# Performance work log

Measured on AMD Instinct MI355X. Metric: run time of the kernel, lower is better.

Reference implementation:

```python
import jax, jax.numpy as jnp
import numpy as np
from jax import lax

B, S, D, T = 64, 256, 1024, 60
HIST = 20  # last-20 window of attn / decoder-state history


def setup_inputs() -> dict:
    key = jax.random.key(0)
    ks = jax.random.split(key, 8)
    e_outputs = jax.random.normal(ks[0], (B, S, D), jnp.float32)
    queries = jax.random.normal(ks[1], (B, T, D), jnp.float32)
    # attention weights over source frames: rows sum to 1
    attns = jax.nn.softmax(jax.random.normal(ks[2], (B, T, S), jnp.float32), axis=-1)
    g = 0.02
    Wr = jax.random.normal(ks[3], (D, 1), jnp.float32) * g
    br = jnp.zeros((1,), jnp.float32)
    Wa = jax.random.normal(ks[4], (D, 1), jnp.float32) * g
    ba = jnp.zeros((1,), jnp.float32)
    Wq = jax.random.normal(ks[5], (D, D), jnp.float32) / np.sqrt(D)
    Wn = jax.random.normal(ks[6], (2 * D, 1), jnp.float32) * g
    bn = jnp.zeros((1,), jnp.float32)
    return {"e_outputs": e_outputs, "queries": queries, "attns": attns,
            "Wr": Wr, "br": br, "Wa": Wa, "ba": ba, "Wq": Wq, "Wn": Wn, "bn": bn}


def reference(e_outputs, queries, attns, Wr, br, Wa, ba, Wq, Wn, bn):
    Bn, Sn, Dn = e_outputs.shape
    # decay1[i] = (i+1)/20 ; decay2[i] = 1-(i+1)/50, zero-padded past 50 frames
    decay1 = (jnp.arange(HIST, dtype=jnp.float32) + 1.0) / 20.0
    idx = jnp.arange(Sn, dtype=jnp.float32)
    add0 = jnp.where(idx < 50, 1.0 - (idx + 1.0) / 50.0, 0.0)
    add_state0 = add0[None, :, None]                       # [1,S,1]
    mem0 = e_outputs * add_state0                          # [B,S,D]
    abuf0 = jnp.zeros((HIST, Bn, Sn), e_outputs.dtype)
    qbuf0 = jnp.zeros((HIST, Bn, Dn), e_outputs.dtype)

    def step(carry, x):
        mem, add_state, abuf, qbuf, i = carry
        attn_i, q_i = x                                    # [B,S], [B,D]
        # read: selected frame before memory update
        sel = jnp.einsum('bs,bsd->bd', attn_i, mem)
        # roll history buffers (newest at slot HIST-1)
        abuf = jnp.concatenate([abuf[1:], attn_i[None]], axis=0)
        qbuf = jnp.concatenate([qbuf[1:], q_i[None]], axis=0)
        k = jnp.minimum(i + 1, HIST)
        valid = jnp.arange(HIST) >= (HIST - k)
        temp = jax.nn.softmax(jnp.where(valid, decay1, -jnp.inf))
        attn_w = jnp.einsum('t,tbs->bs', temp, abuf)       # decayed attn sum
        query_s = jnp.einsum('t,tbd->bd', temp, qbuf)      # decayed query sum
        remove_prob = jax.nn.sigmoid(q_i @ Wr + br)[:, :, None]   # [B,1,1]
        add_prob = jax.nn.sigmoid(q_i @ Wa + ba)[:, :, None]      # [B,1,1]
        sim = jax.nn.sigmoid(jnp.einsum('bsd,bd->bs', mem, query_s @ Wq))[..., None]
        mem = mem * (1.0 - remove_prob * attn_w[..., None] * sim)
        last_ctx = jnp.einsum('bs,bsd->bd', attn_w, e_outputs)[:, None, :]
        cat = jnp.concatenate([e_outputs, jnp.broadcast_to(last_ctx, e_outputs.shape)], axis=-1)
        nxt = jax.nn.sigmoid(cat @ Wn + bn)                # [B,S,1]
        mem = mem + e_outputs * (1.0 - add_state) * (add_prob * nxt)
        add_state = add_state + (1.0 - add_state) * (add_prob * nxt)
        return (mem, add_state, abuf, qbuf, i + 1), sel

    init = (mem0, jnp.broadcast_to(add_state0, (Bn, Sn, 1)), abuf0, qbuf0, jnp.int32(0))
    xs = (attns.transpose(1, 0, 2), queries.transpose(1, 0, 2))
    _, sels = lax.scan(step, init, xs)
    return sels.transpose(1, 0, 2)                         # [B,T,D]
```

## Files before the change

### kernel.cpp

```cpp
#include <hip/hip_runtime.h>
#include <math.h>


#define Bn 64
#define Sn 256
#define Dn 1024
#define Tn 60
#define HISTn 20
#define LDK 72

typedef __bf16 bf16x8 __attribute__((ext_vector_type(8)));
typedef float f32x4 __attribute__((ext_vector_type(4)));
typedef unsigned short us8 __attribute__((ext_vector_type(8)));

__device__ __forceinline__ unsigned short f2bf(float f){
  unsigned int x; __builtin_memcpy(&x,&f,4);
  unsigned int lsb = (x >> 16) & 1u;
  x += 0x7fffu + lsb;
  return (unsigned short)(x >> 16);
}
__device__ __forceinline__ float sigmoidf_(float x){ return 1.0f/(1.0f+expf(-x)); }

__global__ __launch_bounds__(256) void conv_q(
    const float* __restrict__ Q, const float* __restrict__ Wr,
    const float* __restrict__ br, const float* __restrict__ Wa,
    const float* __restrict__ ba, float* __restrict__ rp,
    float* __restrict__ ap, unsigned short* __restrict__ Qbf)
{
  int row = blockIdx.x, tid = threadIdx.x;
  float4 x = ((const float4*)(Q + (size_t)row*Dn))[tid];
  float4 a = ((const float4*)Wr)[tid];
  float4 b = ((const float4*)Wa)[tid];
  unsigned short o[4] = {f2bf(x.x), f2bf(x.y), f2bf(x.z), f2bf(x.w)};
  *(uint2*)&Qbf[(size_t)row*Dn + tid*4] = *(uint2*)o;
  float s1 = x.x*a.x + x.y*a.y + x.z*a.z + x.w*a.w;
  float s2 = x.x*b.x + x.y*b.y + x.z*b.z + x.w*b.w;
  for (int off = 32; off; off >>= 1){
    s1 += __shfl_down(s1, off, 64);
    s2 += __shfl_down(s2, off, 64);
  }
  __shared__ float r1[4], r2[4];
  int lane = tid & 63, wv = tid >> 6;
  if (lane == 0){ r1[wv] = s1; r2[wv] = s2; }
  __syncthreads();
  if (tid == 0){
    rp[row] = sigmoidf_(r1[0]+r1[1]+r1[2]+r1[3] + br[0]);
    ap[row] = sigmoidf_(r2[0]+r2[1]+r2[2]+r2[3] + ba[0]);
  }
}

__global__ __launch_bounds__(256) void conv_wt(
    const float* __restrict__ Wq, unsigned short* __restrict__ WT)
{
  __shared__ __align__(16) unsigned short Tt[64][LDK];
  int n0 = blockIdx.x*64, k0 = blockIdx.y*64;
  int tid = threadIdx.x;
  int kl = tid >> 4, nl4 = (tid & 15)*4;
  #pragma unroll
  for (int it = 0; it < 4; it++){
    int k = kl + it*16;
    float4 v = *(const float4*)&Wq[(size_t)(k0+k)*Dn + n0 + nl4];
    Tt[nl4+0][k] = f2bf(v.x); Tt[nl4+1][k] = f2bf(v.y);
    Tt[nl4+2][k] = f2bf(v.z); Tt[nl4+3][k] = f2bf(v.w);
  }
  __syncthreads();
  int nr = tid >> 2, kg = (tid & 3)*16;
  *(us8*)&WT[(size_t)(n0+nr)*Dn + k0+kg]   = *(us8*)&Tt[nr][kg];
  *(us8*)&WT[(size_t)(n0+nr)*Dn + k0+kg+8] = *(us8*)&Tt[nr][kg+8];
}

__global__ __launch_bounds__(256) void gemm_qw(
    const unsigned short* __restrict__ Qbf,
    const unsigned short* __restrict__ WT,
    unsigned short* __restrict__ QWbf)
{
  __shared__ __align__(16) unsigned short As[64][LDK], Bs[64][LDK];
  int m0 = blockIdx.x*64, n0 = blockIdx.y*64;
  int tid = threadIdx.x, lane = tid & 63, wave = tid >> 6;
  int quad = lane >> 4, l16 = lane & 15;
  f32x4 acc[4];
  #pragma unroll
  for (int nt=0;nt<4;nt++)
    #pragma unroll
    for (int r=0;r<4;r++) acc[nt][r]=0.f;
  int sr = tid >> 2, sk = (tid & 3)*16;
  for (int k0 = 0; k0 < Dn; k0 += 64){
    *(us8*)&As[sr][sk]   = *(const us8*)&Qbf[(size_t)(m0+sr)*Dn + k0+sk];
    *(us8*)&As[sr][sk+8] = *(const us8*)&Qbf[(size_t)(m0+sr)*Dn + k0+sk+8];
    *(us8*)&Bs[sr][sk]   = *(const us8*)&WT[(size_t)(n0+sr)*Dn + k0+sk];
    *(us8*)&Bs[sr][sk+8] = *(const us8*)&WT[(size_t)(n0+sr)*Dn + k0+sk+8];
    __syncthreads();
    #pragma unroll
    for (int kk = 0; kk < 64; kk += 32){
      bf16x8 a = *(const bf16x8*)&As[wave*16 + l16][kk + quad*8];
      #pragma unroll
      for (int nt=0;nt<4;nt++){
        bf16x8 bb = *(const bf16x8*)&Bs[nt*16 + l16][kk + quad*8];
        acc[nt] = __builtin_amdgcn_mfma_f32_16x16x32_bf16(a, bb, acc[nt], 0, 0, 0);
      }
    }
    __syncthreads();
  }
  #pragma unroll
  for (int nt=0;nt<4;nt++)
    #pragma unroll
    for (int r=0;r<4;r++){
      int m = m0 + wave*16 + quad*4 + r;
      int n = n0 + nt*16 + l16;
      QWbf[(size_t)m*Dn + n] = f2bf(acc[nt][r]);
    }
}

__global__ __launch_bounds__(256) void gemm_g(
    const unsigned short* __restrict__ QWbf,
    const float* __restrict__ E,
    const float* __restrict__ Wn,
    float* __restrict__ G, float* __restrict__ eW1, float* __restrict__ eW2)
{
  __shared__ __align__(16) unsigned short As[64][LDK], Bs[32][LDK];
  int b = blockIdx.x, n0 = blockIdx.y*32;
  int tid = threadIdx.x, lane = tid & 63, wave = tid >> 6;
  int quad = lane >> 4, l16 = lane & 15;
  f32x4 acc[2];
  #pragma unroll
  for (int nt=0;nt<2;nt++)
    #pragma unroll
    for (int r=0;r<4;r++) acc[nt][r]=0.f;
  int sr = tid >> 2, sk = (tid & 3)*16;
  int br = tid >> 3, bk = (tid & 7)*8;
  float d1 = 0.f, d2 = 0.f;
  for (int k0 = 0; k0 < Dn; k0 += 64){
    if (sr < Tn){
      *(us8*)&As[sr][sk]   = *(const us8*)&QWbf[((size_t)(b*Tn + sr))*Dn + k0+sk];
      *(us8*)&As[sr][sk+8] = *(const us8*)&QWbf[((size_t)(b*Tn + sr))*Dn + k0+sk+8];
    } else {
      us8 z = (us8)0;
      *(us8*)&As[sr][sk] = z; *(us8*)&As[sr][sk+8] = z;
    }
    const float* ep = &E[((size_t)(b*Sn + n0 + br))*Dn + k0 + bk];
    float4 e0 = *(const float4*)ep;
    float4 e1 = *(const float4*)(ep+4);
    const float* w1 = &Wn[k0 + bk];
    const float* w2 = &Wn[Dn + k0 + bk];
    float4 w10 = *(const float4*)w1, w11 = *(const float4*)(w1+4);
    float4 w20 = *(const float4*)w2, w21 = *(const float4*)(w2+4);
    d1 += e0.x*w10.x + e0.y*w10.y + e0.z*w10.z + e0.w*w10.w
        + e1.x*w11.x + e1.y*w11.y + e1.z*w11.z + e1.w*w11.w;
    d2 += e0.x*w20.x + e0.y*w20.y + e0.z*w20.z + e0.w*w20.w
        + e1.x*w21.x + e1.y*w21.y + e1.z*w21.z + e1.w*w21.w;
    unsigned short cv[8] = {f2bf(e0.x), f2bf(e0.y), f2bf(e0.z), f2bf(e0.w),
                            f2bf(e1.x), f2bf(e1.y), f2bf(e1.z), f2bf(e1.w)};
    *(us8*)&Bs[br][bk] = *(us8*)cv;
    __syncthreads();
    #pragma unroll
    for (int kk = 0; kk < 64; kk += 32){
      bf16x8 a = *(const bf16x8*)&As[wave*16 + l16][kk + quad*8];
      #pragma unroll
      for (int nt=0;nt<2;nt++){
        bf16x8 bb = *(const bf16x8*)&Bs[nt*16 + l16][kk + quad*8];
        acc[nt] = __builtin_amdgcn_mfma_f32_16x16x32_bf16(a, bb, acc[nt], 0, 0, 0);
      }
    }
    __syncthreads();
  }
  d1 += __shfl_down(d1, 4, 64); d1 += __shfl_down(d1, 2, 64); d1 += __shfl_down(d1, 1, 64);
  d2 += __shfl_down(d2, 4, 64); d2 += __shfl_down(d2, 2, 64); d2 += __shfl_down(d2, 1, 64);
  if ((tid & 7) == 0){
    eW1[b*Sn + n0 + br] = d1;
    eW2[b*Sn + n0 + br] = d2;
  }
  #pragma unroll
  for (int nt=0;nt<2;nt++)
    #pragma unroll
    for (int r=0;r<4;r++){
      int t = wave*16 + quad*4 + r;
      int s = n0 + nt*16 + l16;
      if (t < Tn) G[((size_t)(b*Tn + t))*Sn + s] = acc[nt][r];
    }
}

__global__ __launch_bounds__(256) void kR_lc(
    const float* __restrict__ At,
    const float* __restrict__ eW2,
    float* __restrict__ lc)
{
  int b = blockIdx.x, tid = threadIdx.x;
  int lane = tid & 63, wv = tid >> 6;
  __shared__ float Rsh[Tn];
  float4 e2v = ((const float4*)(eW2 + (size_t)b*Sn))[lane];
  const float* at_b = At + (size_t)b*Tn*Sn;
  #pragma unroll
  for (int w = 0; w < 15; w++){
    int j = wv + w*4;
    float4 a4 = ((const float4*)(at_b + (size_t)j*Sn))[lane];
    float v = a4.x*e2v.x + a4.y*e2v.y + a4.z*e2v.z + a4.w*e2v.w;
    #pragma unroll
    for (int off = 32; off; off >>= 1) v += __shfl_down(v, off, 64);
    if (lane == 0) Rsh[j] = v;
  }
  __syncthreads();
  if (tid < Tn){
    int i = tid;
    int j0 = (i - HISTn + 1 > 0) ? i - HISTn + 1 : 0;
    float num = 0.f, den = 0.f;
    for (int j = j0; j <= i; j++){
      float wj = expf(0.05f*(j+1));
      num += wj * Rsh[j];
      den += wj;
    }
    lc[b*Tn + i] = num / den;
  }
}

__global__ __launch_bounds__(256) void scan_m(
    const float* __restrict__ At,
    const float* __restrict__ G,
    const float* __restrict__ rp,
    const float* __restrict__ ap,
    const float* __restrict__ eW1,
    const float* __restrict__ lc,
    const float* __restrict__ bnp,
    unsigned short* __restrict__ Pbf)
{
  int b = blockIdx.x, s = threadIdx.x;
  float M = (s < 50) ? (1.0f - (s+1)/50.0f) : 0.0f;
  float A = M;
  float bnv = bnp[0];
  float e1 = eW1[b*Sn + s];
  const float* at_b = At + (size_t)b*Tn*Sn + s;
  const float* G_b  = G  + (size_t)b*Tn*Sn + s;
  unsigned short* P_b = Pbf + (size_t)b*Tn*Sn + s;
  const float* lc_b = lc + b*Tn;
  const float* rp_b = rp + b*Tn;
  const float* ap_b = ap + b*Tn;
  float num_a = 0.f, num_q = 0.f, den = 0.f;
  #pragma unroll
  for (int i = 0; i < Tn; i++){
    float wi = expf(0.05f*(i+1));
    float a_new = at_b[i*Sn];
    float g_new = G_b[i*Sn];
    num_a += wi * a_new;
    num_q += wi * g_new;
    den   += wi;
    if (i >= HISTn){
      float wo = expf(0.05f*(i-HISTn+1));
      num_a -= wo * at_b[(i-HISTn)*Sn];
      num_q -= wo * G_b[(i-HISTn)*Sn];
      den   -= wo;
    }
    float inv = 1.0f / den;
    float aw = num_a * inv;
    float qd = num_q * inv;
    P_b[i*Sn] = f2bf(a_new * M);
    float sim = sigmoidf_(M * qd);
    float nxt = sigmoidf_(e1 + lc_b[i] + bnv);
    M = M * (1.0f - rp_b[i] * aw * sim);
    float g = (1.0f - A) * ap_b[i] * nxt;
    M += g; A += g;
  }
}

__global__ __launch_bounds__(256) void gemm_sels(
    const unsigned short* __restrict__ Pbf,
    const float* __restrict__ E,
    float* __restrict__ out)
{
  __shared__ __align__(16) unsigned short As[64][LDK], Bs[64][LDK];
  int b = blockIdx.x, n0 = blockIdx.y*64;
  int tid = threadIdx.x, lane = tid & 63, wave = tid >> 6;
  int quad = lane >> 4, l16 = lane & 15;
  f32x4 acc[4];
  #pragma unroll
  for (int nt=0;nt<4;nt++)
    #pragma unroll
    for (int r=0;r<4;r++) acc[nt][r]=0.f;
  int sr = tid >> 2, sk = (tid & 3)*16;
  for (int k0 = 0; k0 < Sn; k0 += 64){
    if (sr < Tn){
      *(us8*)&As[sr][sk]   = *(const us8*)&Pbf[((size_t)(b*Tn + sr))*Sn + k0+sk];
      *(us8*)&As[sr][sk+8] = *(const us8*)&Pbf[((size_t)(b*Tn + sr))*Sn + k0+sk+8];
    } else {
      us8 z = (us8)0;
      *(us8*)&As[sr][sk] = z; *(us8*)&As[sr][sk+8] = z;
    }
    {
      const float* ep = &E[((size_t)(b*Sn + k0 + sr))*Dn + n0 + sk];
      float4 e0 = *(const float4*)ep;
      float4 e1 = *(const float4*)(ep+4);
      float4 e2 = *(const float4*)(ep+8);
      float4 e3 = *(const float4*)(ep+12);
      float ev[16] = {e0.x,e0.y,e0.z,e0.w, e1.x,e1.y,e1.z,e1.w,
                      e2.x,e2.y,e2.z,e2.w, e3.x,e3.y,e3.z,e3.w};
      #pragma unroll
      for (int j=0;j<16;j++) Bs[sk+j][sr] = f2bf(ev[j]);
    }
    __syncthreads();
    #pragma unroll
    for (int kk = 0; kk < 64; kk += 32){
      bf16x8 a = *(const bf16x8*)&As[wave*16 + l16][kk + quad*8];
      #pragma unroll
      for (int nt=0;nt<4;nt++){
        bf16x8 bb = *(const bf16x8*)&Bs[nt*16 + l16][kk + quad*8];
        acc[nt] = __builtin_amdgcn_mfma_f32_16x16x32_bf16(a, bb, acc[nt], 0, 0, 0);
      }
    }
    __syncthreads();
  }
  #pragma unroll
  for (int nt=0;nt<4;nt++)
    #pragma unroll
    for (int r=0;r<4;r++){
      int t = wave*16 + quad*4 + r;
      int d = n0 + nt*16 + l16;
      if (t < Tn) out[((size_t)(b*Tn + t))*Dn + d] = acc[nt][r];
    }
}

extern "C" void kernel_launch(void* const* d_in, const int* in_sizes, int n_in,
                              void* d_out, int out_size, void* d_ws, size_t ws_size,
                              hipStream_t stream)
{
  const float* E  = (const float*)d_in[0];
  const float* Q  = (const float*)d_in[1];
  const float* At = (const float*)d_in[2];
  const float* Wr = (const float*)d_in[3];
  const float* br = (const float*)d_in[4];
  const float* Wa = (const float*)d_in[5];
  const float* ba = (const float*)d_in[6];
  const float* Wq = (const float*)d_in[7];
  const float* Wn = (const float*)d_in[8];
  const float* bnp= (const float*)d_in[9];

  char* ws = (char*)d_ws;
  float* rp  = (float*)ws; ws += (size_t)Bn*Tn*4;
  float* ap  = (float*)ws; ws += (size_t)Bn*Tn*4;
  float* eW1 = (float*)ws; ws += (size_t)Bn*Sn*4;
  float* eW2 = (float*)ws; ws += (size_t)Bn*Sn*4;
  float* lc  = (float*)ws; ws += (size_t)Bn*Tn*4;
  unsigned short* Qbf  = (unsigned short*)ws; ws += (size_t)Bn*Tn*Dn*2;
  unsigned short* WT   = (unsigned short*)ws; ws += (size_t)Dn*Dn*2;
  unsigned short* QWbf = (unsigned short*)ws; ws += (size_t)Bn*Tn*Dn*2;
  float* G = (float*)ws; ws += (size_t)Bn*Tn*Sn*4;
  unsigned short* Pbf = (unsigned short*)ws; ws += (size_t)Bn*Tn*Sn*2;

  conv_q<<<Bn*Tn, 256, 0, stream>>>(Q, Wr, br, Wa, ba, rp, ap, Qbf);
  conv_wt<<<dim3(16,16), 256, 0, stream>>>(Wq, WT);
  gemm_qw<<<dim3(Bn*Tn/64, Dn/64), 256, 0, stream>>>(Qbf, WT, QWbf);
  gemm_g<<<dim3(Bn, Sn/32), 256, 0, stream>>>(QWbf, E, Wn, G, eW1, eW2);
  kR_lc<<<Bn, 256, 0, stream>>>(At, eW2, lc);
  scan_m<<<Bn, 256, 0, stream>>>(At, G, rp, ap, eW1, lc, bnp, Pbf);
  gemm_sels<<<dim3(Bn, Dn/64), 256, 0, stream>>>(Pbf, E, (float*)d_out);
}
```

Before: 220.3 us.

## Pre-convert E to bf16 once and fuse small prep kernels

```diff
diff --git a/kernel.cpp b/kernel.cpp
--- a/kernel.cpp
+++ b/kernel.cpp
@@ -13,6 +13,9 @@
 typedef float f32x4 __attribute__((ext_vector_type(4)));
 typedef unsigned short us8 __attribute__((ext_vector_type(8)));
 
+__device__ __forceinline__ float bf2f(unsigned short u){
+  unsigned int x = ((unsigned int)u) << 16; float f; __builtin_memcpy(&f,&x,4); return f;
+}
 __device__ __forceinline__ unsigned short f2bf(float f){
   unsigned int x; __builtin_memcpy(&x,&f,4);
   unsigned int lsb = (x >> 16) & 1u;
@@ -21,52 +24,61 @@
 }
 __device__ __forceinline__ float sigmoidf_(float x){ return 1.0f/(1.0f+expf(-x)); }
 
-__global__ __launch_bounds__(256) void conv_q(
+__global__ __launch_bounds__(256) void conv_qw(
     const float* __restrict__ Q, const float* __restrict__ Wr,
     const float* __restrict__ br, const float* __restrict__ Wa,
-    const float* __restrict__ ba, float* __restrict__ rp,
-    float* __restrict__ ap, unsigned short* __restrict__ Qbf)
-{
-  int row = blockIdx.x, tid = threadIdx.x;
-  float4 x = ((const float4*)(Q + (size_t)row*Dn))[tid];
-  float4 a = ((const float4*)Wr)[tid];
-  float4 b = ((const float4*)Wa)[tid];
-  unsigned short o[4] = {f2bf(x.x), f2bf(x.y), f2bf(x.z), f2bf(x.w)};
-  *(uint2*)&Qbf[(size_t)row*Dn + tid*4] = *(uint2*)o;
-  float s1 = x.x*a.x + x.y*a.y + x.z*a.z + x.w*a.w;
-  float s2 = x.x*b.x + x.y*b.y + x.z*b.z + x.w*b.w;
-  for (int off = 32; off; off >>= 1){
-    s1 += __shfl_down(s1, off, 64);
-    s2 += __shfl_down(s2, off, 64);
-  }
-  __shared__ float r1[4], r2[4];
-  int lane = tid & 63, wv = tid >> 6;
-  if (lane == 0){ r1[wv] = s1; r2[wv] = s2; }
-  __syncthreads();
-  if (tid == 0){
-    rp[row] = sigmoidf_(r1[0]+r1[1]+r1[2]+r1[3] + br[0]);
-    ap[row] = sigmoidf_(r2[0]+r2[1]+r2[2]+r2[3] + ba[0]);
-  }
-}
-
-__global__ __launch_bounds__(256) void conv_wt(
-    const float* __restrict__ Wq, unsigned short* __restrict__ WT)
-{
-  __shared__ __align__(16) unsigned short Tt[64][LDK];
-  int n0 = blockIdx.x*64, k0 = blockIdx.y*64;
+    const float* __restrict__ ba, const float* __restrict__ Wq,
+    float* __restrict__ rp, float* __restrict__ ap,
+    unsigned short* __restrict__ Qbf, unsigned short* __restrict__ WT)
+{
   int tid = threadIdx.x;
-  int kl = tid >> 4, nl4 = (tid & 15)*4;
-  #pragma unroll
-  for (int it = 0; it < 4; it++){
-    int k = kl + it*16;
-    float4 v = *(const float4*)&Wq[(size_t)(k0+k)*Dn + n0 + nl4];
-    Tt[nl4+0][k] = f2bf(v.x); Tt[nl4+1][k] = f2bf(v.y);
-    Tt[nl4+2][k] = f2bf(v.z); Tt[nl4+3][k] = f2bf(v.w);
-  }
-  __syncthreads();
-  int nr = tid >> 2, kg = (tid & 3)*16;
-  *(us8*)&WT[(size_t)(n0+nr)*Dn + k0+kg]   = *(us8*)&Tt[nr][kg];
-  *(us8*)&WT[(size_t)(n0+nr)*Dn + k0+kg+8] = *(us8*)&Tt[nr][kg+8];
+  if (blockIdx.x < Bn*Tn){
+    int row = blockIdx.x;
+    float4 x = ((const float4*)(Q + (size_t)row*Dn))[tid];
+    float4 a = ((const float4*)Wr)[tid];
+    float4 b = ((const float4*)Wa)[tid];
+    unsigned short o[4] = {f2bf(x.x), f2bf(x.y), f2bf(x.z), f2bf(x.w)};
+    *(uint2*)&Qbf[(size_t)row*Dn + tid*4] = *(uint2*)o;
+    float s1 = x.x*a.x + x.y*a.y + x.z*a.z + x.w*a.w;
+    float s2 = x.x*b.x + x.y*b.y + x.z*b.z + x.w*b.w;
+    for (int off = 32; off; off >>= 1){
+      s1 += __shfl_down(s1, off, 64);
+      s2 += __shfl_down(s2, off, 64);
+    }
+    __shared__ float r1[4], r2[4];
+    int lane = tid & 63, wv = tid >> 6;
+    if (lane == 0){ r1[wv] = s1; r2[wv] = s2; }
+    __syncthreads();
+    if (tid == 0){
+      rp[row] = sigmoidf_(r1[0]+r1[1]+r1[2]+r1[3] + br[0]);
+      ap[row] = sigmoidf_(r2[0]+r2[1]+r2[2]+r2[3] + ba[0]);
+    }
+  } else {
+    __shared__ __align__(16) unsigned short Tt[64][LDK];
+    int t = blockIdx.x - Bn*Tn;
+    int n0 = (t >> 4)*64, k0 = (t & 15)*64;
+    int kl = tid >> 4, nl4 = (tid & 15)*4;
+    #pragma unroll
+    for (int it = 0; it < 4; it++){
+      int k = kl + it*16;
+      float4 v = *(const float4*)&Wq[(size_t)(k0+k)*Dn + n0 + nl4];
+      Tt[nl4+0][k] = f2bf(v.x); Tt[nl4+1][k] = f2bf(v.y);
+      Tt[nl4+2][k] = f2bf(v.z); Tt[nl4+3][k] = f2bf(v.w);
+    }
+    __syncthreads();
+    int nr = tid >> 2, kg = (tid & 3)*16;
+    *(us8*)&WT[(size_t)(n0+nr)*Dn + k0+kg]   = *(us8*)&Tt[nr][kg];
+    *(us8*)&WT[(size_t)(n0+nr)*Dn + k0+kg+8] = *(us8*)&Tt[nr][kg+8];
+  }
+}
+
+__global__ __launch_bounds__(256) void conv_e(
+    const float* __restrict__ E, unsigned short* __restrict__ Ebf)
+{
+  size_t i = (size_t)blockIdx.x*256 + threadIdx.x;
+  float4 v = ((const float4*)E)[i];
+  unsigned short o[4] = {f2bf(v.x), f2bf(v.y), f2bf(v.z), f2bf(v.w)};
+  ((uint2*)Ebf)[i] = *(uint2*)o;
 }
 
 __global__ __launch_bounds__(256) void gemm_qw(
@@ -113,7 +125,7 @@
 
 __global__ __launch_bounds__(256) void gemm_g(
     const unsigned short* __restrict__ QWbf,
-    const float* __restrict__ E,
+    const unsigned short* __restrict__ Ebf,
     const float* __restrict__ Wn,
     float* __restrict__ G, float* __restrict__ eW1, float* __restrict__ eW2)
 {
@@ -127,7 +139,7 @@
     #pragma unroll
     for (int r=0;r<4;r++) acc[nt][r]=0.f;
   int sr = tid >> 2, sk = (tid & 3)*16;
-  int br = tid >> 3, bk = (tid & 7)*8;
+  int brw = tid >> 3, bk = (tid & 7)*8;
   float d1 = 0.f, d2 = 0.f;
   for (int k0 = 0; k0 < Dn; k0 += 64){
     if (sr < Tn){
@@ -137,20 +149,18 @@
       us8 z = (us8)0;
       *(us8*)&As[sr][sk] = z; *(us8*)&As[sr][sk+8] = z;
     }
-    const float* ep = &E[((size_t)(b*Sn + n0 + br))*Dn + k0 + bk];
-    float4 e0 = *(const float4*)ep;
-    float4 e1 = *(const float4*)(ep+4);
-    const float* w1 = &Wn[k0 + bk];
-    const float* w2 = &Wn[Dn + k0 + bk];
-    float4 w10 = *(const float4*)w1, w11 = *(const float4*)(w1+4);
-    float4 w20 = *(const float4*)w2, w21 = *(const float4*)(w2+4);
-    d1 += e0.x*w10.x + e0.y*w10.y + e0.z*w10.z + e0.w*w10.w
-        + e1.x*w11.x + e1.y*w11.y + e1.z*w11.z + e1.w*w11.w;
-    d2 += e0.x*w20.x + e0.y*w20.y + e0.z*w20.z + e0.w*w20.w
-        + e1.x*w21.x + e1.y*w21.y + e1.z*w21.z + e1.w*w21.w;
-    unsigned short cv[8] = {f2bf(e0.x), f2bf(e0.y), f2bf(e0.z), f2bf(e0.w),
-                            f2bf(e1.x), f2bf(e1.y), f2bf(e1.z), f2bf(e1.w)};
-    *(us8*)&Bs[br][bk] = *(us8*)cv;
+    us8 ev = *(const us8*)&Ebf[((size_t)(b*Sn + n0 + brw))*Dn + k0 + bk];
+    *(us8*)&Bs[brw][bk] = ev;
+    float4 w10 = *(const float4*)&Wn[k0 + bk];
+    float4 w11 = *(const float4*)&Wn[k0 + bk + 4];
+    float4 w20 = *(const float4*)&Wn[Dn + k0 + bk];
+    float4 w21 = *(const float4*)&Wn[Dn + k0 + bk + 4];
+    float e0 = bf2f(ev[0]), e1 = bf2f(ev[1]), e2 = bf2f(ev[2]), e3 = bf2f(ev[3]);
+    float e4 = bf2f(ev[4]), e5 = bf2f(ev[5]), e6 = bf2f(ev[6]), e7 = bf2f(ev[7]);
+    d1 += e0*w10.x + e1*w10.y + e2*w10.z + e3*w10.w
+        + e4*w11.x + e5*w11.y + e6*w11.z + e7*w11.w;
+    d2 += e0*w20.x + e1*w20.y + e2*w20.z + e3*w20.w
+        + e4*w21.x + e5*w21.y + e6*w21.z + e7*w21.w;
     __syncthreads();
     #pragma unroll
     for (int kk = 0; kk < 64; kk += 32){
@@ -166,8 +176,8 @@
   d1 += __shfl_down(d1, 4, 64); d1 += __shfl_down(d1, 2, 64); d1 += __shfl_down(d1, 1, 64);
   d2 += __shfl_down(d2, 4, 64); d2 += __shfl_down(d2, 2, 64); d2 += __shfl_down(d2, 1, 64);
   if ((tid & 7) == 0){
-    eW1[b*Sn + n0 + br] = d1;
-    eW2[b*Sn + n0 + br] = d2;
+    eW1[b*Sn + n0 + brw] = d1;
+    eW2[b*Sn + n0 + brw] = d2;
   }
   #pragma unroll
   for (int nt=0;nt<2;nt++)
@@ -179,20 +189,25 @@
     }
 }
 
-__global__ __launch_bounds__(256) void kR_lc(
+__global__ __launch_bounds__(256) void scan_m(
     const float* __restrict__ At,
+    const float* __restrict__ G,
+    const float* __restrict__ rp,
+    const float* __restrict__ ap,
+    const float* __restrict__ eW1,
     const float* __restrict__ eW2,
-    float* __restrict__ lc)
+    const float* __restrict__ bnp,
+    unsigned short* __restrict__ Pbf)
 {
   int b = blockIdx.x, tid = threadIdx.x;
   int lane = tid & 63, wv = tid >> 6;
-  __shared__ float Rsh[Tn];
+  __shared__ float Rsh[Tn], lcs[Tn];
   float4 e2v = ((const float4*)(eW2 + (size_t)b*Sn))[lane];
-  const float* at_b = At + (size_t)b*Tn*Sn;
+  const float* at_base = At + (size_t)b*Tn*Sn;
   #pragma unroll
   for (int w = 0; w < 15; w++){
     int j = wv + w*4;
-    float4 a4 = ((const float4*)(at_b + (size_t)j*Sn))[lane];
+    float4 a4 = ((const float4*)(at_base + (size_t)j*Sn))[lane];
     float v = a4.x*e2v.x + a4.y*e2v.y + a4.z*e2v.z + a4.w*e2v.w;
     #pragma unroll
     for (int off = 32; off; off >>= 1) v += __shfl_down(v, off, 64);
@@ -208,21 +223,10 @@
       num += wj * Rsh[j];
       den += wj;
     }
-    lc[b*Tn + i] = num / den;
-  }
-}
-
-__global__ __launch_bounds__(256) void scan_m(
-    const float* __restrict__ At,
-    const float* __restrict__ G,
-    const float* __restrict__ rp,
-    const float* __restrict__ ap,
-    const float* __restrict__ eW1,
-    const float* __restrict__ lc,
-    const float* __restrict__ bnp,
-    unsigned short* __restrict__ Pbf)
-{
-  int b = blockIdx.x, s = threadIdx.x;
+    lcs[i] = num / den;
+  }
+  __syncthreads();
+  int s = tid;
   float M = (s < 50) ? (1.0f - (s+1)/50.0f) : 0.0f;
   float A = M;
   float bnv = bnp[0];
@@ -230,7 +234,6 @@
   const float* at_b = At + (size_t)b*Tn*Sn + s;
   const float* G_b  = G  + (size_t)b*Tn*Sn + s;
   unsigned short* P_b = Pbf + (size_t)b*Tn*Sn + s;
-  const float* lc_b = lc + b*Tn;
   const float* rp_b = rp + b*Tn;
   const float* ap_b = ap + b*Tn;
   float num_a = 0.f, num_q = 0.f, den = 0.f;
@@ -253,7 +256,7 @@
     float qd = num_q * inv;
     P_b[i*Sn] = f2bf(a_new * M);
     float sim = sigmoidf_(M * qd);
-    float nxt = sigmoidf_(e1 + lc_b[i] + bnv);
+    float nxt = sigmoidf_(e1 + lcs[i] + bnv);
     M = M * (1.0f - rp_b[i] * aw * sim);
     float g = (1.0f - A) * ap_b[i] * nxt;
     M += g; A += g;
@@ -262,7 +265,7 @@
 
 __global__ __launch_bounds__(256) void gemm_sels(
     const unsigned short* __restrict__ Pbf,
-    const float* __restrict__ E,
+    const unsigned short* __restrict__ Ebf,
     float* __restrict__ out)
 {
   __shared__ __align__(16) unsigned short As[64][LDK], Bs[64][LDK];
@@ -284,15 +287,14 @@
       *(us8*)&As[sr][sk] = z; *(us8*)&As[sr][sk+8] = z;
     }
     {
-      const float* ep = &E[((size_t)(b*Sn + k0 + sr))*Dn + n0 + sk];
-      float4 e0 = *(const float4*)ep;
-      float4 e1 = *(const float4*)(ep+4);
-      float4 e2 = *(const float4*)(ep+8);
-      float4 e3 = *(const float4*)(ep+12);
-      float ev[16] = {e0.x,e0.y,e0.z,e0.w, e1.x,e1.y,e1.z,e1.w,
-                      e2.x,e2.y,e2.z,e2.w, e3.x,e3.y,e3.z,e3.w};
+      const unsigned short* ep = &Ebf[((size_t)(b*Sn + k0 + sr))*Dn + n0 + sk];
+      us8 e0 = *(const us8*)ep;
+      us8 e1 = *(const us8*)(ep + 8);
       #pragma unroll
-      for (int j=0;j<16;j++) Bs[sk+j][sr] = f2bf(ev[j]);
+      for (int j=0;j<8;j++){
+        Bs[sk+j][sr]   = e0[j];
+        Bs[sk+8+j][sr] = e1[j];
+      }
     }
     __syncthreads();
     #pragma unroll
@@ -336,18 +338,17 @@
   float* ap  = (float*)ws; ws += (size_t)Bn*Tn*4;
   float* eW1 = (float*)ws; ws += (size_t)Bn*Sn*4;
   float* eW2 = (float*)ws; ws += (size_t)Bn*Sn*4;
-  float* lc  = (float*)ws; ws += (size_t)Bn*Tn*4;
   unsigned short* Qbf  = (unsigned short*)ws; ws += (size_t)Bn*Tn*Dn*2;
   unsigned short* WT   = (unsigned short*)ws; ws += (size_t)Dn*Dn*2;
   unsigned short* QWbf = (unsigned short*)ws; ws += (size_t)Bn*Tn*Dn*2;
+  unsigned short* Ebf  = (unsigned short*)ws; ws += (size_t)Bn*Sn*Dn*2;
   float* G = (float*)ws; ws += (size_t)Bn*Tn*Sn*4;
   unsigned short* Pbf = (unsigned short*)ws; ws += (size_t)Bn*Tn*Sn*2;
 
-  conv_q<<<Bn*Tn, 256, 0, stream>>>(Q, Wr, br, Wa, ba, rp, ap, Qbf);
-  conv_wt<<<dim3(16,16), 256, 0, stream>>>(Wq, WT);
+  conv_qw<<<Bn*Tn + 256, 256, 0, stream>>>(Q, Wr, br, Wa, ba, Wq, rp, ap, Qbf, WT);
+  conv_e<<<(Bn*Sn*Dn/4)/256, 256, 0, stream>>>(E, Ebf);
   gemm_qw<<<dim3(Bn*Tn/64, Dn/64), 256, 0, stream>>>(Qbf, WT, QWbf);
-  gemm_g<<<dim3(Bn, Sn/32), 256, 0, stream>>>(QWbf, E, Wn, G, eW1, eW2);
-  kR_lc<<<Bn, 256, 0, stream>>>(At, eW2, lc);
-  scan_m<<<Bn, 256, 0, stream>>>(At, G, rp, ap, eW1, lc, bnp, Pbf);
-  gemm_sels<<<dim3(Bn, Dn/64), 256, 0, stream>>>(Pbf, E, (float*)d_out);
-}
+  gemm_g<<<dim3(Bn, Sn/32), 256, 0, stream>>>(QWbf, Ebf, Wn, G, eW1, eW2);
+  scan_m<<<Bn, 256, 0, stream>>>(At, G, rp, ap, eW1, eW2, bnp, Pbf);
+  gemm_sels<<<dim3(Bn, Dn/64), 256, 0, stream>>>(Pbf, Ebf, (float*)d_out);
+}
```

New measurement: 212.8 us. 1.04x faster.
